# Performance work log

Hardware: AMD Instinct MI355X
Metric: run time of the kernel (lower is better)

## Reference

```python
import jax, jax.numpy as jnp
import numpy as np

K_NUM = 3


def setup_inputs() -> dict:
    key = jax.random.key(0)
    k1, k2, k3, k4 = jax.random.split(key, 4)
    n, c_in, t, v = 16, 64, 2048, 25
    c_out = 64
    x = jax.random.normal(k1, (n, c_in, t, v), dtype=jnp.float32)
    A_skl = jax.random.uniform(k2, (K_NUM, v, v), dtype=jnp.float32)
    # nn.Linear(in_channels, out_channels * k_num): weight [k*c_out, c_in], bias [k*c_out]
    W = jax.random.normal(k3, (K_NUM * c_out, c_in), dtype=jnp.float32) * (1.0 / np.sqrt(c_in))
    b = jax.random.normal(k4, (K_NUM * c_out,), dtype=jnp.float32) * 0.01
    return {"x": x, "A_skl": A_skl, "W": W, "b": b}


def reference(x, A_skl, W, b):
    n, c_in, t, v = x.shape
    kc = W.shape[0]
    c_out = kc // K_NUM
    # permute -> Linear -> permute back, fused into one einsum over channels:
    # h[n, k*c_out, t, v] = sum_c W[o, c] * x[n, c, t, v] + b[o]
    h = jnp.einsum('nctv,oc->notv', x, W) + b[None, :, None, None]
    # view(n, k, c_out, t, v): channel dim splits as (k major, c_out minor)
    h = h.reshape(n, K_NUM, c_out, t, v)
    # graph aggregation over k adjacency subsets
    out = jnp.einsum('nkctv,kvw->nctw', h, A_skl)
    return out
```

## Files before the change

### kernel.cpp

```cpp
#include <hip/hip_runtime.h>


typedef short short8 __attribute__((ext_vector_type(8)));
typedef float floatx4 __attribute__((ext_vector_type(4)));
typedef unsigned int uintx4 __attribute__((ext_vector_type(4)));

#define K_NUM 3
#define C_IN  64
#define C_OUT 64
#define T_DIM 2048
#define V_DIM 25
#define N_DIM 16

#define TT    2
#define NSUB  16
#define TWIN  32
#define XROW  51200

#define WBUF_ELEMS (12*2*64*8)
#define ABUF_OFF   (WBUF_ELEMS*2)
#define ABUF_ELEMS (3*2*64*8)
#define B2_OFF     (ABUF_OFF + ABUF_ELEMS*2)
#define B2_ELEMS   (4*2*64*4)

__device__ __forceinline__ unsigned short bf16_rne(float f) {
    unsigned int u = __builtin_bit_cast(unsigned int, f);
    unsigned int r = (u + 0x7FFFu + ((u >> 16) & 1u)) >> 16;
    return (unsigned short)r;
}
__device__ __forceinline__ unsigned int pack_rh(float fx, float fy) {
    unsigned int ux = __builtin_bit_cast(unsigned int, fx);
    unsigned int uy = __builtin_bit_cast(unsigned int, fy);
    return ((ux + 0x8000u) >> 16) | ((uy + 0x8000u) & 0xFFFF0000u);
}

__global__ void sgcn_prep(const float* __restrict__ W, const float* __restrict__ A,
                          const float* __restrict__ b,
                          unsigned short* __restrict__ wbuf,
                          unsigned short* __restrict__ abuf,
                          float* __restrict__ b2buf) {
    int idx = blockIdx.x * 256 + threadIdx.x;
    if (idx < WBUF_ELEMS) {
        int j = idx & 7, lane = (idx >> 3) & 63, ks = (idx >> 9) & 1, nt = idx >> 10;
        int o  = nt * 16 + (lane & 15);
        int ci = ks * 32 + ((lane >> 4) & 3) * 8 + j;
        wbuf[idx] = bf16_rne(W[o * C_IN + ci]);
    }
    if (idx < ABUF_ELEMS) {
        int j = idx & 7, lane = (idx >> 3) & 63, nt = (idx >> 9) & 1, k = idx >> 10;
        int w = nt * 16 + (lane & 15);
        int v = ((lane >> 4) & 3) * 8 + j;
        abuf[idx] = (v < V_DIM && w < V_DIM) ? bf16_rne(A[(k * V_DIM + v) * V_DIM + w])
                                             : (unsigned short)0;
    }
    if (idx < B2_ELEMS) {
        int r = idx & 3, lane = (idx >> 2) & 63, nt = (idx >> 8) & 1, mt2 = idx >> 9;
        int c = mt2 * 16 + ((lane >> 4) & 3) * 4 + r;
        int w = nt * 16 + (lane & 15);
        float val = 0.f;
        if (w < V_DIM) {
            for (int k = 0; k < K_NUM; ++k) {
                float cs = 0.f;
                for (int v = 0; v < V_DIM; ++v) cs += A[(k * V_DIM + v) * V_DIM + w];
                val += b[k * C_OUT + c] * cs;
            }
        }
        b2buf[idx] = val;
    }
}

__global__ __launch_bounds__(512)
void sgcn_main(const float* __restrict__ x,
               const unsigned short* __restrict__ wbuf,
               const unsigned short* __restrict__ abuf,
               const float* __restrict__ b2buf,
               float* __restrict__ out) {
    __shared__ __align__(16) unsigned int   Xt[2][64 * 32];
    __shared__ __align__(16) unsigned short H2[2][K_NUM * TT * 64 * 32];

    const int tid  = threadIdx.x;
    const int lane = tid & 63;
    const int wid  = tid >> 6;
    const int nb   = blockIdx.x >> 6;
    const int t_base = (blockIdx.x & 63) * TWIN;

    const int wm2 = wid & 1;
    const int wq  = wid >> 1;
    const int mt2 = wid & 3, th = wid >> 2;

    short8 wfr[3][2];
    #pragma unroll
    for (int ni = 0; ni < 3; ++ni)
        #pragma unroll
        for (int ks = 0; ks < 2; ++ks)
            wfr[ni][ks] = ((const short8*)wbuf)[(((wq * 3 + ni) * 2 + ks) * 64) + lane];
    short8 afr2[3][2];
    #pragma unroll
    for (int k = 0; k < 3; ++k)
        #pragma unroll
        for (int nt = 0; nt < 2; ++nt)
            afr2[k][nt] = ((const short8*)abuf)[((k * 2 + nt) * 64) + lane];
    floatx4 b2f[2];
    b2f[0] = reinterpret_cast<const floatx4*>(b2buf)[(mt2 * 2 + 0) * 64 + lane];
    b2f[1] = reinterpret_cast<const floatx4*>(b2buf)[(mt2 * 2 + 1) * 64 + lane];

    for (int i = tid; i < 2 * 14 * 32; i += 512) {
        int bsel = i >= 14 * 32;
        int j = i - bsel * 14 * 32;
        int pc = j >> 5, ciw = j & 31;
        int col = (pc < 7) ? (25 + pc) : (50 + pc);
        Xt[bsel][col * 32 + ciw] = 0u;
    }

    float xq[8];
    const float* xptr = x + ((size_t)nb * C_IN * T_DIM + t_base) * V_DIM;
    const int ciq = tid / 50, cg = tid % 50;
    const int icol = (cg / 25) * 32 + (cg % 25);
    const int isw  = (ciq ^ ((icol >> 1) & 7)) * 4;

    auto LOADX = [&](int ts) {
        if (tid < 400) {
            const float* s = xptr + ts * (TT * V_DIM) + (size_t)(ciq * 8) * XROW + cg;
            #pragma unroll
            for (int r = 0; r < 8; ++r) xq[r] = s[(size_t)r * XROW];
        }
    };
    auto WRITEX = [&](int bsel) {
        if (tid < 400) {
            uintx4 pk;
            #pragma unroll
            for (int j = 0; j < 4; ++j)
                pk[j] = pack_rh(xq[2 * j], xq[2 * j + 1]);
            *reinterpret_cast<uintx4*>(&Xt[bsel][icol * 32 + isw]) = pk;
        }
    };

    LOADX(0);
    WRITEX(0);
    LOADX(1);

    #pragma unroll 1
    for (int ts = 0; ts <= NSUB; ++ts) {
        __syncthreads();
        const int cur = ts & 1, prv = 1 - cur;

        floatx4 acc1[2][3];
        short8 xfr[2][2];
        if (ts < NSUB) {
            #pragma unroll
            for (int mi = 0; mi < 2; ++mi) {
                int acol = (wm2 * 2 + mi) * 16 + (lane & 15);
                #pragma unroll
                for (int ks = 0; ks < 2; ++ks) {
                    int blk = (ks * 4 + ((lane >> 4) & 3)) ^ ((acol >> 1) & 7);
                    xfr[mi][ks] = *(const short8*)&Xt[cur][acol * 32 + blk * 4];
                }
            }
        }

        short8 ha[3];
        if (ts >= 1) {
            const int c_a = mt2 * 16 + (lane & 15);
            #pragma unroll
            for (int k = 0; k < K_NUM; ++k) {
                int row = (k * TT + th) * 64 + c_a;
                int blk = ((lane >> 4) & 3) ^ ((c_a >> 2) & 3);
                ha[k] = *(const short8*)&((const unsigned int*)H2[prv])[row * 16 + blk * 4];
            }
        }

        if (ts + 1 < NSUB) WRITEX(cur ^ 1);
        if (ts + 2 < NSUB) LOADX(ts + 2);

        if (ts < NSUB) {
            #pragma unroll
            for (int mi = 0; mi < 2; ++mi)
                #pragma unroll
                for (int ni = 0; ni < 3; ++ni)
                    acc1[mi][ni] = floatx4{0.f, 0.f, 0.f, 0.f};
            #pragma unroll
            for (int mi = 0; mi < 2; ++mi)
                #pragma unroll
                for (int ni = 0; ni < 3; ++ni)
                    #pragma unroll
                    for (int ks = 0; ks < 2; ++ks)
                        acc1[mi][ni] = __builtin_amdgcn_mfma_f32_16x16x32_bf16(
                            xfr[mi][ks], wfr[ni][ks], acc1[mi][ni], 0, 0, 0);

            #pragma unroll
            for (int mi = 0; mi < 2; ++mi) {
                int vb = mi * 16 + ((lane >> 4) & 3) * 4;
                #pragma unroll
                for (int ni = 0; ni < 3; ++ni) {
                    int o = wq * 48 + ni * 16 + (lane & 15);
                    int k = o >> 6, c = o & 63;
                    int swv = vb ^ (((c >> 2) & 3) << 3);
                    unsigned long long lo = pack_rh(acc1[mi][ni][0], acc1[mi][ni][1]);
                    unsigned long long hi = pack_rh(acc1[mi][ni][2], acc1[mi][ni][3]);
                    int idx16 = ((k * TT + wm2) * 64 + c) * 32 + swv;
                    ((unsigned long long*)H2[cur])[idx16 >> 2] = lo | (hi << 32);
                }
            }
        }

        if (ts >= 1) {
            floatx4 acc2[2];
            acc2[0] = b2f[0];
            acc2[1] = b2f[1];
            #pragma unroll
            for (int k = 0; k < K_NUM; ++k)
                #pragma unroll
                for (int nt = 0; nt < 2; ++nt)
                    acc2[nt] = __builtin_amdgcn_mfma_f32_16x16x32_bf16(
                        ha[k], afr2[k][nt], acc2[nt], 0, 0, 0);

            const int tg = t_base + (ts - 1) * TT + th;
            const int c0 = mt2 * 16 + ((lane >> 4) & 3) * 4;
            const int wl = lane & 15;
            #pragma unroll
            for (int r = 0; r < 4; ++r)
                out[((size_t)(nb * C_OUT + c0 + r) * T_DIM + tg) * V_DIM + wl] = acc2[0][r];
            if (wl < 9) {
                #pragma unroll
                for (int r = 0; r < 4; ++r)
                    out[((size_t)(nb * C_OUT + c0 + r) * T_DIM + tg) * V_DIM + 16 + wl] = acc2[1][r];
            }
        }
    }
}

extern "C" void kernel_launch(void* const* d_in, const int* in_sizes, int n_in,
                              void* d_out, int out_size, void* d_ws, size_t ws_size,
                              hipStream_t stream) {
    const float* x = (const float*)d_in[0];
    const float* A = (const float*)d_in[1];
    const float* W = (const float*)d_in[2];
    const float* b = (const float*)d_in[3];
    float* out = (float*)d_out;

    unsigned short* wbuf = (unsigned short*)d_ws;
    unsigned short* abuf = (unsigned short*)((char*)d_ws + ABUF_OFF);
    float* b2buf = (float*)((char*)d_ws + B2_OFF);

    sgcn_prep<<<(WBUF_ELEMS + 255) / 256, 256, 0, stream>>>(W, A, b, wbuf, abuf, b2buf);

    dim3 grid(N_DIM * (T_DIM / TWIN));
    sgcn_main<<<grid, 512, 0, stream>>>(x, wbuf, abuf, b2buf, out);
}
```

Baseline: 121.4 us.

## Restructure main kernel into independent per-wave time slices without block barriers

Each wave now owns a contiguous run of four time steps and keeps private LDS buffers, so the block-wide __syncthreads pipeline is gone. Per time step a wave stages x in fp32, converts it to bf16 fragments, then computes all three k subsets itself before aggregating with the adjacency. Weights and A fragments are reloaded from global or L1 inside the loop instead of being held in registers. Blocks shrink to 256 threads and the grid doubles. The aim is to drop cross-wave synchronization, at the cost of scalar global staging loads, more LDS traffic and repeated weight fetches.

```diff
diff --git a/kernel.cpp b/kernel.cpp
--- a/kernel.cpp
+++ b/kernel.cpp
@@ -11,13 +11,12 @@
 #define T_DIM 2048
 #define V_DIM 25
 #define N_DIM 16
-
-#define TT    2
-#define NSUB  16
-#define TWIN  32
-#define XROW  51200
-
-#define WBUF_ELEMS (12*2*64*8)
+#define XROW  (T_DIM * V_DIM)
+
+#define TW    4
+#define TWIN  16
+
+#define WBUF_ELEMS (3*4*2*64*8)
 #define ABUF_OFF   (WBUF_ELEMS*2)
 #define ABUF_ELEMS (3*2*64*8)
 #define B2_OFF     (ABUF_OFF + ABUF_ELEMS*2)
@@ -41,8 +40,9 @@
                           float* __restrict__ b2buf) {
     int idx = blockIdx.x * 256 + threadIdx.x;
     if (idx < WBUF_ELEMS) {
-        int j = idx & 7, lane = (idx >> 3) & 63, ks = (idx >> 9) & 1, nt = idx >> 10;
-        int o  = nt * 16 + (lane & 15);
+        int j = idx & 7, lane = (idx >> 3) & 63, ks = (idx >> 9) & 1;
+        int ni = (idx >> 10) & 3, k = idx >> 12;
+        int o  = k * 64 + ni * 16 + (lane & 15);
         int ci = ks * 32 + ((lane >> 4) & 3) * 8 + j;
         wbuf[idx] = bf16_rne(W[o * C_IN + ci]);
     }
@@ -54,8 +54,8 @@
                                              : (unsigned short)0;
     }
     if (idx < B2_ELEMS) {
-        int r = idx & 3, lane = (idx >> 2) & 63, nt = (idx >> 8) & 1, mt2 = idx >> 9;
-        int c = mt2 * 16 + ((lane >> 4) & 3) * 4 + r;
+        int r = idx & 3, lane = (idx >> 2) & 63, nt = (idx >> 8) & 1, mt = idx >> 9;
+        int c = mt * 16 + ((lane >> 4) & 3) * 4 + r;
         int w = nt * 16 + (lane & 15);
         float val = 0.f;
         if (w < V_DIM) {
@@ -69,161 +69,134 @@
     }
 }
 
-__global__ __launch_bounds__(512)
+__global__ __launch_bounds__(256)
 void sgcn_main(const float* __restrict__ x,
                const unsigned short* __restrict__ wbuf,
                const unsigned short* __restrict__ abuf,
                const float* __restrict__ b2buf,
                float* __restrict__ out) {
-    __shared__ __align__(16) unsigned int   Xt[2][64 * 32];
-    __shared__ __align__(16) unsigned short H2[2][K_NUM * TT * 64 * 32];
+    __shared__ __align__(16) float          xs[4][1664];
+    __shared__ __align__(16) unsigned short hs[4][64 * 32];
 
     const int tid  = threadIdx.x;
     const int lane = tid & 63;
     const int wid  = tid >> 6;
-    const int nb   = blockIdx.x >> 6;
-    const int t_base = (blockIdx.x & 63) * TWIN;
-
-    const int wm2 = wid & 1;
-    const int wq  = wid >> 1;
-    const int mt2 = wid & 3, th = wid >> 2;
-
-    short8 wfr[3][2];
-    #pragma unroll
-    for (int ni = 0; ni < 3; ++ni)
-        #pragma unroll
-        for (int ks = 0; ks < 2; ++ks)
-            wfr[ni][ks] = ((const short8*)wbuf)[(((wq * 3 + ni) * 2 + ks) * 64) + lane];
-    short8 afr2[3][2];
-    #pragma unroll
-    for (int k = 0; k < 3; ++k)
-        #pragma unroll
-        for (int nt = 0; nt < 2; ++nt)
-            afr2[k][nt] = ((const short8*)abuf)[((k * 2 + nt) * 64) + lane];
-    floatx4 b2f[2];
-    b2f[0] = reinterpret_cast<const floatx4*>(b2buf)[(mt2 * 2 + 0) * 64 + lane];
-    b2f[1] = reinterpret_cast<const floatx4*>(b2buf)[(mt2 * 2 + 1) * 64 + lane];
-
-    for (int i = tid; i < 2 * 14 * 32; i += 512) {
-        int bsel = i >= 14 * 32;
-        int j = i - bsel * 14 * 32;
-        int pc = j >> 5, ciw = j & 31;
-        int col = (pc < 7) ? (25 + pc) : (50 + pc);
-        Xt[bsel][col * 32 + ciw] = 0u;
-    }
-
-    float xq[8];
-    const float* xptr = x + ((size_t)nb * C_IN * T_DIM + t_base) * V_DIM;
-    const int ciq = tid / 50, cg = tid % 50;
-    const int icol = (cg / 25) * 32 + (cg % 25);
-    const int isw  = (ciq ^ ((icol >> 1) & 7)) * 4;
-
-    auto LOADX = [&](int ts) {
-        if (tid < 400) {
-            const float* s = xptr + ts * (TT * V_DIM) + (size_t)(ciq * 8) * XROW + cg;
-            #pragma unroll
-            for (int r = 0; r < 8; ++r) xq[r] = s[(size_t)r * XROW];
+    const int nb   = blockIdx.x >> 7;
+    const int t0   = (blockIdx.x & 127) * TWIN + wid * TW;
+
+    float* xw = xs[wid];
+    unsigned short* hw = hs[wid];
+
+    const short8*  wbuf8 = (const short8*)wbuf;
+    const short8*  abuf8 = (const short8*)abuf;
+    const floatx4* b2b4  = (const floatx4*)b2buf;
+    const float*   xbase = x + (size_t)nb * C_IN * XROW;
+
+    xw[1600 + lane] = 0.f;
+
+    const int kg = (lane >> 4) & 3;
+    const int ln = lane & 15;
+
+    auto STAGE = [&](int t) {
+        #pragma unroll
+        for (int i = 0; i < 25; ++i) {
+            int u  = i * 64 + lane;
+            int ci = u / 25, v = u - ci * 25;
+            xw[u] = xbase[(size_t)ci * XROW + t * V_DIM + v];
         }
     };
-    auto WRITEX = [&](int bsel) {
-        if (tid < 400) {
-            uintx4 pk;
-            #pragma unroll
-            for (int j = 0; j < 4; ++j)
-                pk[j] = pack_rh(xq[2 * j], xq[2 * j + 1]);
-            *reinterpret_cast<uintx4*>(&Xt[bsel][icol * 32 + isw]) = pk;
-        }
-    };
-
-    LOADX(0);
-    WRITEX(0);
-    LOADX(1);
+
+    STAGE(t0);
 
     #pragma unroll 1
-    for (int ts = 0; ts <= NSUB; ++ts) {
-        __syncthreads();
-        const int cur = ts & 1, prv = 1 - cur;
-
-        floatx4 acc1[2][3];
+    for (int j = 0; j < TW; ++j) {
+        const int t = t0 + j;
+
         short8 xfr[2][2];
-        if (ts < NSUB) {
+        #pragma unroll
+        for (int mi = 0; mi < 2; ++mi) {
+            const int v = mi * 16 + ln;
+            #pragma unroll
+            for (int ks = 0; ks < 2; ++ks) {
+                const int cib = ks * 32 + kg * 8;
+                float f0 = xw[(cib + 0) * 25 + v], f1 = xw[(cib + 1) * 25 + v];
+                float f2 = xw[(cib + 2) * 25 + v], f3 = xw[(cib + 3) * 25 + v];
+                float f4 = xw[(cib + 4) * 25 + v], f5 = xw[(cib + 5) * 25 + v];
+                float f6 = xw[(cib + 6) * 25 + v], f7 = xw[(cib + 7) * 25 + v];
+                uintx4 p;
+                p[0] = pack_rh(f0, f1); p[1] = pack_rh(f2, f3);
+                p[2] = pack_rh(f4, f5); p[3] = pack_rh(f6, f7);
+                xfr[mi][ks] = __builtin_bit_cast(short8, p);
+            }
+        }
+
+        if (j + 1 < TW) STAGE(t + 1);
+
+        floatx4 acc2[4][2];
+        #pragma unroll
+        for (int mt = 0; mt < 4; ++mt)
+            #pragma unroll
+            for (int nt = 0; nt < 2; ++nt)
+                acc2[mt][nt] = b2b4[(mt * 2 + nt) * 64 + lane];
+
+        #pragma unroll
+        for (int k = 0; k < K_NUM; ++k) {
+            floatx4 acc1[2][4];
+            #pragma unroll
+            for (int mi = 0; mi < 2; ++mi)
+                #pragma unroll
+                for (int ni = 0; ni < 4; ++ni)
+                    acc1[mi][ni] = floatx4{0.f, 0.f, 0.f, 0.f};
+
+            #pragma unroll
+            for (int ks = 0; ks < 2; ++ks)
+                #pragma unroll
+                for (int ni = 0; ni < 4; ++ni) {
+                    short8 wf = wbuf8[((k * 4 + ni) * 2 + ks) * 64 + lane];
+                    #pragma unroll
+                    for (int mi = 0; mi < 2; ++mi)
+                        acc1[mi][ni] = __builtin_amdgcn_mfma_f32_16x16x32_bf16(
+                            xfr[mi][ks], wf, acc1[mi][ni], 0, 0, 0);
+                }
+
             #pragma unroll
             for (int mi = 0; mi < 2; ++mi) {
-                int acol = (wm2 * 2 + mi) * 16 + (lane & 15);
-                #pragma unroll
-                for (int ks = 0; ks < 2; ++ks) {
-                    int blk = (ks * 4 + ((lane >> 4) & 3)) ^ ((acol >> 1) & 7);
-                    xfr[mi][ks] = *(const short8*)&Xt[cur][acol * 32 + blk * 4];
-                }
-            }
-        }
-
-        short8 ha[3];
-        if (ts >= 1) {
-            const int c_a = mt2 * 16 + (lane & 15);
-            #pragma unroll
-            for (int k = 0; k < K_NUM; ++k) {
-                int row = (k * TT + th) * 64 + c_a;
-                int blk = ((lane >> 4) & 3) ^ ((c_a >> 2) & 3);
-                ha[k] = *(const short8*)&((const unsigned int*)H2[prv])[row * 16 + blk * 4];
-            }
-        }
-
-        if (ts + 1 < NSUB) WRITEX(cur ^ 1);
-        if (ts + 2 < NSUB) LOADX(ts + 2);
-
-        if (ts < NSUB) {
-            #pragma unroll
-            for (int mi = 0; mi < 2; ++mi)
-                #pragma unroll
-                for (int ni = 0; ni < 3; ++ni)
-                    acc1[mi][ni] = floatx4{0.f, 0.f, 0.f, 0.f};
-            #pragma unroll
-            for (int mi = 0; mi < 2; ++mi)
-                #pragma unroll
-                for (int ni = 0; ni < 3; ++ni)
-                    #pragma unroll
-                    for (int ks = 0; ks < 2; ++ks)
-                        acc1[mi][ni] = __builtin_amdgcn_mfma_f32_16x16x32_bf16(
-                            xfr[mi][ks], wfr[ni][ks], acc1[mi][ni], 0, 0, 0);
-
-            #pragma unroll
-            for (int mi = 0; mi < 2; ++mi) {
-                int vb = mi * 16 + ((lane >> 4) & 3) * 4;
-                #pragma unroll
-                for (int ni = 0; ni < 3; ++ni) {
-                    int o = wq * 48 + ni * 16 + (lane & 15);
-                    int k = o >> 6, c = o & 63;
-                    int swv = vb ^ (((c >> 2) & 3) << 3);
+                const int vb = mi * 16 + kg * 4;
+                #pragma unroll
+                for (int ni = 0; ni < 4; ++ni) {
+                    const int c   = ni * 16 + ln;
+                    const int swv = vb ^ (((c >> 2) & 3) << 3);
                     unsigned long long lo = pack_rh(acc1[mi][ni][0], acc1[mi][ni][1]);
                     unsigned long long hi = pack_rh(acc1[mi][ni][2], acc1[mi][ni][3]);
-                    int idx16 = ((k * TT + wm2) * 64 + c) * 32 + swv;
-                    ((unsigned long long*)H2[cur])[idx16 >> 2] = lo | (hi << 32);
+                    ((unsigned long long*)hw)[(c * 32 + swv) >> 2] = lo | (hi << 32);
                 }
             }
-        }
-
-        if (ts >= 1) {
-            floatx4 acc2[2];
-            acc2[0] = b2f[0];
-            acc2[1] = b2f[1];
-            #pragma unroll
-            for (int k = 0; k < K_NUM; ++k)
-                #pragma unroll
-                for (int nt = 0; nt < 2; ++nt)
-                    acc2[nt] = __builtin_amdgcn_mfma_f32_16x16x32_bf16(
-                        ha[k], afr2[k][nt], acc2[nt], 0, 0, 0);
-
-            const int tg = t_base + (ts - 1) * TT + th;
-            const int c0 = mt2 * 16 + ((lane >> 4) & 3) * 4;
-            const int wl = lane & 15;
-            #pragma unroll
-            for (int r = 0; r < 4; ++r)
-                out[((size_t)(nb * C_OUT + c0 + r) * T_DIM + tg) * V_DIM + wl] = acc2[0][r];
-            if (wl < 9) {
-                #pragma unroll
-                for (int r = 0; r < 4; ++r)
-                    out[((size_t)(nb * C_OUT + c0 + r) * T_DIM + tg) * V_DIM + 16 + wl] = acc2[1][r];
+
+            short8 ha[4];
+            #pragma unroll
+            for (int mt = 0; mt < 4; ++mt) {
+                const int c_a = mt * 16 + ln;
+                const int blk = kg ^ ((c_a >> 2) & 3);
+                ha[mt] = *(const short8*)&((const unsigned int*)hw)[c_a * 16 + blk * 4];
+            }
+            #pragma unroll
+            for (int nt = 0; nt < 2; ++nt) {
+                short8 af = abuf8[(k * 2 + nt) * 64 + lane];
+                #pragma unroll
+                for (int mt = 0; mt < 4; ++mt)
+                    acc2[mt][nt] = __builtin_amdgcn_mfma_f32_16x16x32_bf16(
+                        ha[mt], af, acc2[mt][nt], 0, 0, 0);
+            }
+        }
+
+        #pragma unroll
+        for (int mt = 0; mt < 4; ++mt) {
+            const int c0 = mt * 16 + kg * 4;
+            #pragma unroll
+            for (int r = 0; r < 4; ++r) {
+                float* ob = out + ((size_t)(nb * C_OUT + c0 + r) * T_DIM + t) * V_DIM;
+                ob[ln] = acc2[mt][0][r];
+                if (ln < 9) ob[16 + ln] = acc2[mt][1][r];
             }
         }
     }
@@ -245,5 +218,5 @@
     sgcn_prep<<<(WBUF_ELEMS + 255) / 256, 256, 0, stream>>>(W, A, b, wbuf, abuf, b2buf);
 
     dim3 grid(N_DIM * (T_DIM / TWIN));
-    sgcn_main<<<grid, 512, 0, stream>>>(x, wbuf, abuf, b2buf, out);
-}
+    sgcn_main<<<grid, 256, 0, stream>>>(x, wbuf, abuf, b2buf, out);
+}
```

Result: slower. 271.4 us (+123.5%).
